# Kernel optimization log

Measured on AMD Instinct MI355X. Metric: run time of the kernel, lower is better.

The kernel has to match this reference:

```python
import jax, jax.numpy as jnp
import numpy as np

HIDDEN = 1024
N_HEADS = 16
HEAD_DIM = 64
LOCAL_WINDOW = 1024
GLOBAL_STRIDE = 512


def _sparse_mask(seq_len):
    # local sliding window (half-window each side), strided global columns, causal
    i = jnp.arange(seq_len)[:, None]
    j = jnp.arange(seq_len)[None, :]
    diff = i - j
    local = jnp.abs(diff) <= (LOCAL_WINDOW // 2)
    glob = (j % GLOBAL_STRIDE) == 0
    causal = diff >= 0
    return (local | glob) & causal  # [S, S] bool


def setup_inputs() -> dict:
    key = jax.random.key(0)
    k0, k1, k2, k3, k4 = jax.random.split(key, 5)
    B, S = 1, 2048
    scale = 1.0 / np.sqrt(HIDDEN)
    return {
        "hidden_states": jax.random.normal(k0, (B, S, HIDDEN), dtype=jnp.float32),
        "w_q": jax.random.normal(k1, (HIDDEN, N_HEADS * HEAD_DIM), dtype=jnp.float32) * scale,
        "w_k": jax.random.normal(k2, (HIDDEN, N_HEADS * HEAD_DIM), dtype=jnp.float32) * scale,
        "w_v": jax.random.normal(k3, (HIDDEN, N_HEADS * HEAD_DIM), dtype=jnp.float32) * scale,
        "w_o": jax.random.normal(k4, (N_HEADS * HEAD_DIM, HIDDEN), dtype=jnp.float32) * scale,
    }


def reference(hidden_states, w_q, w_k, w_v, w_o):
    B, S, _ = hidden_states.shape

    def shape(x):  # [B,S,H*D] -> [B,H,S,D]
        return x.reshape(B, S, N_HEADS, HEAD_DIM).transpose(0, 2, 1, 3)

    q = shape(hidden_states @ w_q)
    k = shape(hidden_states @ w_k)
    v = shape(hidden_states @ w_v)

    scores = jnp.einsum("bhqd,bhkd->bhqk", q, k) / np.sqrt(HEAD_DIM)
    mask = _sparse_mask(S)  # [S,S]
    scores = jnp.where(mask[None, None], scores, -jnp.inf)
    attn = jax.nn.softmax(scores, axis=-1)
    out = jnp.einsum("bhqk,bhkd->bhqd", attn, v)
    out = out.transpose(0, 2, 1, 3).reshape(B, S, N_HEADS * HEAD_DIM)
    return out @ w_o
```

## Files before the change

### kernel.cpp

```cpp
#include <hip/hip_runtime.h>

#define SEQ 2048
#define HID 1024
#define NH 16
#define HD 64
#define QKVLD 3072

typedef __attribute__((ext_vector_type(8))) short bf16x8;
typedef __attribute__((ext_vector_type(4))) float f32x4;

__device__ __forceinline__ unsigned short f2bf(float f) {
  unsigned int x = __float_as_uint(f);
  x += 0x7fffu + ((x >> 16) & 1u);
  return (unsigned short)(x >> 16);
}

__device__ __forceinline__ float bf2f(unsigned short u) {
  return __uint_as_float(((unsigned int)u) << 16);
}

__device__ __forceinline__ void gld_lds16(const void* g, void* l) {
  __builtin_amdgcn_global_load_lds((__attribute__((address_space(1))) void*)g,
                                   (__attribute__((address_space(3))) void*)l, 16, 0, 0);
}

__global__ void prep(const float* __restrict__ X, const float* __restrict__ Wq,
                     const float* __restrict__ Wk, const float* __restrict__ Wv,
                     const float* __restrict__ Wo, unsigned short* __restrict__ Xb,
                     unsigned short* __restrict__ WtQKV, unsigned short* __restrict__ WtO) {
  const int z = blockIdx.z;
  if (z == 4) {
    int bid = blockIdx.y * 32 + blockIdx.x;
    int t = threadIdx.y * 32 + threadIdx.x;
    size_t base = (size_t)bid * 2048 + t * 4;
#pragma unroll
    for (int half = 0; half < 2; half++) {
      float4 v = *(const float4*)(X + base + half * 1024);
      ushort4 o;
      o.x = f2bf(v.x); o.y = f2bf(v.y); o.z = f2bf(v.z); o.w = f2bf(v.w);
      *(ushort4*)(Xb + base + half * 1024) = o;
    }
    return;
  }
  __shared__ float tile[32][33];
  const float* S = (z == 0) ? Wq : (z == 1) ? Wk : (z == 2) ? Wv : Wo;
  unsigned short* D = (z < 3) ? (WtQKV + (size_t)z * HID * HID) : WtO;
  const float scale = (z == 0) ? 0.125f : 1.0f;
  int r0 = blockIdx.y * 32, c0 = blockIdx.x * 32;
  int tx = threadIdx.x, ty = threadIdx.y;
#pragma unroll
  for (int k = 0; k < 4; k++)
    tile[ty + k * 8][tx] = S[(size_t)(r0 + ty + k * 8) * HID + c0 + tx];
  __syncthreads();
#pragma unroll
  for (int k = 0; k < 4; k++)
    D[(size_t)(c0 + ty + k * 8) * HID + r0 + tx] = f2bf(scale * tile[tx][ty + k * 8]);
}

template <int MI, int BN, int GX, int RW, int OUT>
__global__ __launch_bounds__(256, 2) void gemm_bt(const unsigned short* __restrict__ A,
                                                  const unsigned short* __restrict__ Bt,
                                                  void* __restrict__ Cout,
                                                  unsigned short* __restrict__ Vout,
                                                  int M, int N, int K) {
  constexpr int NI = BN / 32;
  constexpr int TM = MI * 32;
  __shared__ unsigned short As[TM * 128];
  __shared__ unsigned short Bs[BN * 128];
  const int tid = threadIdx.x;
  const int lane = tid & 63;
  const int w = tid >> 6;
  const int wm = w >> 1, wn = w & 1;
  const int quad = lane >> 4, l16 = lane & 15;

  const int lin = blockIdx.x + GX * blockIdx.y;
  const int xcd = lin & 7, idx = lin >> 3;
  const int bx = (xcd & 3) * RW + (idx % RW);
  const int by = (xcd >> 2) * (64 / RW) + (idx / RW);
  const int bm = by * TM, bn = bx * BN;

  f32x4 acc[MI][NI] = {};

  for (int k0 = 0; k0 < K; k0 += 128) {
#pragma unroll
    for (int c = tid; c < TM * 16; c += 256) {
      int r = c >> 4, kc = c & 15;
      int g = (kc & 12) + ((kc & 3) ^ (r & 3));
      gld_lds16(A + (size_t)(bm + r) * K + k0 + g * 8, As + c * 8);
    }
#pragma unroll
    for (int c = tid; c < BN * 16; c += 256) {
      int r = c >> 4, kc = c & 15;
      int g = (kc & 12) + ((kc & 3) ^ (r & 3));
      gld_lds16(Bt + (size_t)(bn + r) * K + k0 + g * 8, Bs + c * 8);
    }
    __syncthreads();
#pragma unroll
    for (int ks = 0; ks < 4; ks++) {
      bf16x8 af[MI], bfr[NI];
#pragma unroll
      for (int mi = 0; mi < MI; mi++) {
        int m = wm * (MI * 16) + mi * 16 + l16;
        af[mi] = *(const bf16x8*)(As + (m * 16 + ks * 4 + (quad ^ (m & 3))) * 8);
      }
#pragma unroll
      for (int ni = 0; ni < NI; ni++) {
        int n = wn * (BN / 2) + ni * 16 + l16;
        bfr[ni] = *(const bf16x8*)(Bs + (n * 16 + ks * 4 + (quad ^ (n & 3))) * 8);
      }
#pragma unroll
      for (int mi = 0; mi < MI; mi++)
#pragma unroll
        for (int ni = 0; ni < NI; ni++)
          acc[mi][ni] = __builtin_amdgcn_mfma_f32_16x16x32_bf16(af[mi], bfr[ni], acc[mi][ni], 0, 0, 0);
    }
    __syncthreads();
  }

#pragma unroll
  for (int mi = 0; mi < MI; mi++) {
#pragma unroll
    for (int ni = 0; ni < NI; ni++) {
      int row = bm + wm * (MI * 16) + mi * 16 + quad * 4;
      int col = bn + wn * (BN / 2) + ni * 16 + l16;
      if (OUT == 0) {
#pragma unroll
        for (int r = 0; r < 4; r++)
          ((float*)Cout)[(size_t)(row + r) * N + col] = acc[mi][ni][r];
      } else {
        if (col < 2 * HID) {
#pragma unroll
          for (int r = 0; r < 4; r++)
            ((unsigned short*)Cout)[(size_t)(row + r) * N + col] = f2bf(acc[mi][ni][r]);
        } else {
          ushort4 o;
          o.x = f2bf(acc[mi][ni][0]); o.y = f2bf(acc[mi][ni][1]);
          o.z = f2bf(acc[mi][ni][2]); o.w = f2bf(acc[mi][ni][3]);
          *(ushort4*)(Vout + (size_t)(col - 2 * HID) * SEQ + row) = o;
        }
      }
    }
  }
}

__global__ __launch_bounds__(256, 4) void attn_sparse(const unsigned short* __restrict__ QKV,
                                                      const unsigned short* __restrict__ VtG,
                                                      unsigned short* __restrict__ AttO) {
  __shared__ unsigned short Ks[64 * 64];
  __shared__ unsigned short Vt[64 * 64];
  __shared__ unsigned short Pw[4][16 * 72];
  const int lin = blockIdx.x + 32 * blockIdx.y;
  const int xcd = lin & 7, slot = lin >> 3;
  const int h = slot >> 2;
  const int qbase = (xcd * 4 + (slot & 3)) * 64;
  const int tid = threadIdx.x;
  const int lane = tid & 63, w = tid >> 6;
  const int quad = lane >> 4, l16 = lane & 15;
  const int qrow0 = qbase + w * 16;
  unsigned short* pws = &Pw[w][0];

  bf16x8 aq[2];
  {
    const unsigned short* qp = QKV + (size_t)(qrow0 + l16) * QKVLD + h * HD + quad * 8;
    aq[0] = *(const bf16x8*)qp;
    aq[1] = *(const bf16x8*)(qp + 32);
  }

  f32x4 accO[4] = {};
  float lsum = 0.f;

  const int jlo = (qbase >= 512) ? (qbase - 512) : 0;
  const int ng = (jlo > 0) ? ((jlo + 511) >> 9) : 0;
  const int ntl = ((qbase - jlo) >> 6) + 1;

  for (int t = 0; t < ntl; t++) {
    const int j0 = jlo + t * 64;
    if (t > 0) __syncthreads();
#pragma unroll
    for (int c = tid; c < 512; c += 256) {
      int r = c >> 3, kc = c & 7;
      int g = (kc & 4) + ((kc & 3) ^ (r & 3));
      gld_lds16(QKV + (size_t)(j0 + r) * QKVLD + HID + h * HD + g * 8, Ks + c * 8);
      gld_lds16(VtG + (size_t)(h * HD + r) * SEQ + j0 + g * 8, Vt + c * 8);
    }
    __syncthreads();

    f32x4 s[4] = {};
#pragma unroll
    for (int nj = 0; nj < 4; nj++) {
      int row = nj * 16 + l16;
#pragma unroll
      for (int ks = 0; ks < 2; ks++) {
        bf16x8 ak = *(const bf16x8*)(Ks + (row * 8 + ks * 4 + (quad ^ (row & 3))) * 8);
        s[nj] = __builtin_amdgcn_mfma_f32_16x16x32_bf16(ak, aq[ks], s[nj], 0, 0, 0);
      }
    }

    const bool isdiag = (t == ntl - 1);
    const bool istrail = (t == 0) && (qbase >= 512);
    const int trailg = (istrail && ((j0 & 511) == 0)) ? 1 : 0;
    const int db = qrow0 + l16 - j0 - quad * 4;
#pragma unroll
    for (int nj = 0; nj < 4; nj++) {
      float p[4];
#pragma unroll
      for (int r = 0; r < 4; r++) {
        float x = fminf(s[nj][r], 60.0f);
        int d = db - nj * 16 - r;
        bool valid = true;
        if (isdiag) valid = (d >= 0);
        else if (istrail) valid = (d <= 512) || (trailg && (nj * 16 + quad * 4 + r) == 0);
        x = valid ? x : -1e30f;
        p[r] = __expf(x);
        lsum += p[r];
      }
      unsigned int u01 = (unsigned)f2bf(p[0]) | ((unsigned)f2bf(p[1]) << 16);
      unsigned int u23 = (unsigned)f2bf(p[2]) | ((unsigned)f2bf(p[3]) << 16);
      *(uint2*)(pws + l16 * 72 + nj * 16 + quad * 4) = make_uint2(u01, u23);
    }

#pragma unroll
    for (int kk = 0; kk < 2; kk++) {
      bf16x8 bp = *(const bf16x8*)(pws + l16 * 72 + kk * 32 + quad * 8);
#pragma unroll
      for (int nd = 0; nd < 4; nd++) {
        int row = nd * 16 + l16;
        bf16x8 av = *(const bf16x8*)(Vt + (row * 8 + kk * 4 + (quad ^ (row & 3))) * 8);
        accO[nd] = __builtin_amdgcn_mfma_f32_16x16x32_bf16(av, bp, accO[nd], 0, 0, 0);
      }
    }
  }

  if (ng > 0) {
    __syncthreads();
    if (tid < ng * 8) {
      int r = tid >> 3, kc = tid & 7;
      int g = (kc & 4) + ((kc & 3) ^ (r & 3));
      *(uint4*)(Ks + tid * 8) =
          *(const uint4*)(QKV + ((size_t)r << 9) * QKVLD + HID + h * HD + g * 8);
    }
    if (tid < ng * 64) {
      int d = tid & 63, c = tid >> 6;
      Vt[(d * 8 + (d & 3)) * 8 + c] = VtG[(size_t)(h * HD + d) * SEQ + ((size_t)c << 9)];
    }
    __syncthreads();
    f32x4 s0 = {};
#pragma unroll
    for (int ks = 0; ks < 2; ks++) {
      bf16x8 ak = *(const bf16x8*)(Ks + (l16 * 8 + ks * 4 + (quad ^ (l16 & 3))) * 8);
      s0 = __builtin_amdgcn_mfma_f32_16x16x32_bf16(ak, aq[ks], s0, 0, 0, 0);
    }
    float p[4];
#pragma unroll
    for (int r = 0; r < 4; r++) {
      p[r] = ((quad * 4 + r) < ng) ? __expf(fminf(s0[r], 60.0f)) : 0.f;
      lsum += p[r];
    }
    unsigned int u01 = (unsigned)f2bf(p[0]) | ((unsigned)f2bf(p[1]) << 16);
    unsigned int u23 = (unsigned)f2bf(p[2]) | ((unsigned)f2bf(p[3]) << 16);
    *(uint2*)(pws + l16 * 72 + quad * 4) = make_uint2(u01, u23);
    *(uint2*)(pws + l16 * 72 + 16 + quad * 4) = make_uint2(0, 0);
    bf16x8 bp = *(const bf16x8*)(pws + l16 * 72 + quad * 8);
#pragma unroll
    for (int nd = 0; nd < 4; nd++) {
      int row = nd * 16 + l16;
      bf16x8 av = *(const bf16x8*)(Vt + (row * 8 + (quad ^ (row & 3))) * 8);
      accO[nd] = __builtin_amdgcn_mfma_f32_16x16x32_bf16(av, bp, accO[nd], 0, 0, 0);
    }
  }

  lsum += __shfl_xor(lsum, 16);
  lsum += __shfl_xor(lsum, 32);
  const float rl = 1.0f / lsum;
  const int i = qrow0 + l16;
#pragma unroll
  for (int nd = 0; nd < 4; nd++) {
    ushort4 o;
    o.x = f2bf(accO[nd][0] * rl);
    o.y = f2bf(accO[nd][1] * rl);
    o.z = f2bf(accO[nd][2] * rl);
    o.w = f2bf(accO[nd][3] * rl);
    *(ushort4*)(AttO + (size_t)i * HID + h * HD + nd * 16 + quad * 4) = o;
  }
}

extern "C" void kernel_launch(void* const* d_in, const int* in_sizes, int n_in,
                              void* d_out, int out_size, void* d_ws, size_t ws_size,
                              hipStream_t stream) {
  const float* X  = (const float*)d_in[0];
  const float* Wq = (const float*)d_in[1];
  const float* Wk = (const float*)d_in[2];
  const float* Wv = (const float*)d_in[3];
  const float* Wo = (const float*)d_in[4];
  float* out = (float*)d_out;

  unsigned short* Xb    = (unsigned short*)d_ws;
  unsigned short* WtQKV = Xb + (size_t)SEQ * HID;
  unsigned short* WtO   = WtQKV + (size_t)QKVLD * HID;
  unsigned short* QKV   = WtO + (size_t)HID * HID;
  unsigned short* VtG   = QKV + (size_t)SEQ * QKVLD;
  unsigned short* AttO  = VtG + (size_t)HID * SEQ;

  prep<<<dim3(32, 32, 5), dim3(32, 8), 0, stream>>>(X, Wq, Wk, Wv, Wo, Xb, WtQKV, WtO);

  gemm_bt<4, 96, 32, 8, 2><<<dim3(32, 16), dim3(256), 0, stream>>>(
      Xb, WtQKV, QKV, VtG, SEQ, QKVLD, HID);

  attn_sparse<<<dim3(SEQ / 64, NH), dim3(256), 0, stream>>>(QKV, VtG, AttO);

  gemm_bt<2, 64, 16, 4, 0><<<dim3(16, 32), dim3(256), 0, stream>>>(
      AttO, WtO, out, nullptr, SEQ, HID, HID);
}
```

Before: 128.4 us.

## Double-buffer K/V tiles in sparse attention and use packed bf16 conversion

The sparse attention kernel now keeps two LDS buffers for K and V and issues the async global-to-LDS loads for the next tile before computing on the current one, so load latency can overlap with the MFMA work. That needs double the K/V shared memory, and launch bounds drop from 4 to 3 blocks per CU to match. Manual bf16 rounding is replaced with the packed __float22bfloat162_rn intrinsic in several places, and the fminf clamp before exp is removed. The loop-end sync has no matching wait on the async loads, so correctness depends on how the compiler orders that memory traffic, and a stray self-assignment to Ks[0][0] was added.

```diff
diff --git a/kernel.cpp b/kernel.cpp
--- a/kernel.cpp
+++ b/kernel.cpp
@@ -1,4 +1,5 @@
 #include <hip/hip_runtime.h>
+#include <hip/hip_bf16.h>
 
 #define SEQ 2048
 #define HID 1024
@@ -15,8 +16,10 @@
   return (unsigned short)(x >> 16);
 }
 
-__device__ __forceinline__ float bf2f(unsigned short u) {
-  return __uint_as_float(((unsigned int)u) << 16);
+__device__ __forceinline__ unsigned int pkbf(float a, float b) {
+  union { __hip_bfloat162 h2; unsigned int u; } cvt;
+  cvt.h2 = __float22bfloat162_rn(make_float2(a, b));
+  return cvt.u;
 }
 
 __device__ __forceinline__ void gld_lds16(const void* g, void* l) {
@@ -36,9 +39,7 @@
 #pragma unroll
     for (int half = 0; half < 2; half++) {
       float4 v = *(const float4*)(X + base + half * 1024);
-      ushort4 o;
-      o.x = f2bf(v.x); o.y = f2bf(v.y); o.z = f2bf(v.z); o.w = f2bf(v.w);
-      *(ushort4*)(Xb + base + half * 1024) = o;
+      *(uint2*)(Xb + base + half * 1024) = make_uint2(pkbf(v.x, v.y), pkbf(v.z, v.w));
     }
     return;
   }
@@ -133,21 +134,20 @@
           for (int r = 0; r < 4; r++)
             ((unsigned short*)Cout)[(size_t)(row + r) * N + col] = f2bf(acc[mi][ni][r]);
         } else {
-          ushort4 o;
-          o.x = f2bf(acc[mi][ni][0]); o.y = f2bf(acc[mi][ni][1]);
-          o.z = f2bf(acc[mi][ni][2]); o.w = f2bf(acc[mi][ni][3]);
-          *(ushort4*)(Vout + (size_t)(col - 2 * HID) * SEQ + row) = o;
+          *(uint2*)(Vout + (size_t)(col - 2 * HID) * SEQ + row) =
+              make_uint2(pkbf(acc[mi][ni][0], acc[mi][ni][1]),
+                         pkbf(acc[mi][ni][2], acc[mi][ni][3]));
         }
       }
     }
   }
 }
 
-__global__ __launch_bounds__(256, 4) void attn_sparse(const unsigned short* __restrict__ QKV,
+__global__ __launch_bounds__(256, 3) void attn_sparse(const unsigned short* __restrict__ QKV,
                                                       const unsigned short* __restrict__ VtG,
                                                       unsigned short* __restrict__ AttO) {
-  __shared__ unsigned short Ks[64 * 64];
-  __shared__ unsigned short Vt[64 * 64];
+  __shared__ unsigned short Ks[2][64 * 64];
+  __shared__ unsigned short Vt[2][64 * 64];
   __shared__ unsigned short Pw[4][16 * 72];
   const int lin = blockIdx.x + 32 * blockIdx.y;
   const int xcd = lin & 7, slot = lin >> 3;
@@ -173,17 +173,24 @@
   const int ng = (jlo > 0) ? ((jlo + 511) >> 9) : 0;
   const int ntl = ((qbase - jlo) >> 6) + 1;
 
-  for (int t = 0; t < ntl; t++) {
-    const int j0 = jlo + t * 64;
-    if (t > 0) __syncthreads();
+  auto stage = [&](int j0, int b) {
 #pragma unroll
     for (int c = tid; c < 512; c += 256) {
       int r = c >> 3, kc = c & 7;
       int g = (kc & 4) + ((kc & 3) ^ (r & 3));
-      gld_lds16(QKV + (size_t)(j0 + r) * QKVLD + HID + h * HD + g * 8, Ks + c * 8);
-      gld_lds16(VtG + (size_t)(h * HD + r) * SEQ + j0 + g * 8, Vt + c * 8);
-    }
-    __syncthreads();
+      gld_lds16(QKV + (size_t)(j0 + r) * QKVLD + HID + h * HD + g * 8, &Ks[b][c * 8]);
+      gld_lds16(VtG + (size_t)(h * HD + r) * SEQ + j0 + g * 8, &Vt[b][c * 8]);
+    }
+  };
+
+  stage(jlo, 0);
+  __syncthreads();
+
+  for (int t = 0; t < ntl; t++) {
+    if (t + 1 < ntl) stage(jlo + (t + 1) * 64, (t + 1) & 1);
+    const unsigned short* KsB = Ks[t & 1];
+    const unsigned short* VtB = Vt[t & 1];
+    const int j0 = jlo + t * 64;
 
     f32x4 s[4] = {};
 #pragma unroll
@@ -191,7 +198,7 @@
       int row = nj * 16 + l16;
 #pragma unroll
       for (int ks = 0; ks < 2; ks++) {
-        bf16x8 ak = *(const bf16x8*)(Ks + (row * 8 + ks * 4 + (quad ^ (row & 3))) * 8);
+        bf16x8 ak = *(const bf16x8*)(KsB + (row * 8 + ks * 4 + (quad ^ (row & 3))) * 8);
         s[nj] = __builtin_amdgcn_mfma_f32_16x16x32_bf16(ak, aq[ks], s[nj], 0, 0, 0);
       }
     }
@@ -205,7 +212,7 @@
       float p[4];
 #pragma unroll
       for (int r = 0; r < 4; r++) {
-        float x = fminf(s[nj][r], 60.0f);
+        float x = s[nj][r];
         int d = db - nj * 16 - r;
         bool valid = true;
         if (isdiag) valid = (d >= 0);
@@ -214,9 +221,8 @@
         p[r] = __expf(x);
         lsum += p[r];
       }
-      unsigned int u01 = (unsigned)f2bf(p[0]) | ((unsigned)f2bf(p[1]) << 16);
-      unsigned int u23 = (unsigned)f2bf(p[2]) | ((unsigned)f2bf(p[3]) << 16);
-      *(uint2*)(pws + l16 * 72 + nj * 16 + quad * 4) = make_uint2(u01, u23);
+      *(uint2*)(pws + l16 * 72 + nj * 16 + quad * 4) =
+          make_uint2(pkbf(p[0], p[1]), pkbf(p[2], p[3]));
     }
 
 #pragma unroll
@@ -225,46 +231,45 @@
 #pragma unroll
       for (int nd = 0; nd < 4; nd++) {
         int row = nd * 16 + l16;
-        bf16x8 av = *(const bf16x8*)(Vt + (row * 8 + kk * 4 + (quad ^ (row & 3))) * 8);
+        bf16x8 av = *(const bf16x8*)(VtB + (row * 8 + kk * 4 + (quad ^ (row & 3))) * 8);
         accO[nd] = __builtin_amdgcn_mfma_f32_16x16x32_bf16(av, bp, accO[nd], 0, 0, 0);
       }
     }
+    __syncthreads();
   }
 
   if (ng > 0) {
-    __syncthreads();
     if (tid < ng * 8) {
       int r = tid >> 3, kc = tid & 7;
       int g = (kc & 4) + ((kc & 3) ^ (r & 3));
-      *(uint4*)(Ks + tid * 8) =
+      *(uint4*)(&Ks[0][tid * 8]) =
           *(const uint4*)(QKV + ((size_t)r << 9) * QKVLD + HID + h * HD + g * 8);
     }
     if (tid < ng * 64) {
       int d = tid & 63, c = tid >> 6;
-      Vt[(d * 8 + (d & 3)) * 8 + c] = VtG[(size_t)(h * HD + d) * SEQ + ((size_t)c << 9)];
+      Ks[0][0] = Ks[0][0];
+      Vt[0][(d * 8 + (d & 3)) * 8 + c] = VtG[(size_t)(h * HD + d) * SEQ + ((size_t)c << 9)];
     }
     __syncthreads();
     f32x4 s0 = {};
 #pragma unroll
     for (int ks = 0; ks < 2; ks++) {
-      bf16x8 ak = *(const bf16x8*)(Ks + (l16 * 8 + ks * 4 + (quad ^ (l16 & 3))) * 8);
+      bf16x8 ak = *(const bf16x8*)(&Ks[0][(l16 * 8 + ks * 4 + (quad ^ (l16 & 3))) * 8]);
       s0 = __builtin_amdgcn_mfma_f32_16x16x32_bf16(ak, aq[ks], s0, 0, 0, 0);
     }
     float p[4];
 #pragma unroll
     for (int r = 0; r < 4; r++) {
-      p[r] = ((quad * 4 + r) < ng) ? __expf(fminf(s0[r], 60.0f)) : 0.f;
+      p[r] = ((quad * 4 + r) < ng) ? __expf(s0[r]) : 0.f;
       lsum += p[r];
     }
-    unsigned int u01 = (unsigned)f2bf(p[0]) | ((unsigned)f2bf(p[1]) << 16);
-    unsigned int u23 = (unsigned)f2bf(p[2]) | ((unsigned)f2bf(p[3]) << 16);
-    *(uint2*)(pws + l16 * 72 + quad * 4) = make_uint2(u01, u23);
+    *(uint2*)(pws + l16 * 72 + quad * 4) = make_uint2(pkbf(p[0], p[1]), pkbf(p[2], p[3]));
     *(uint2*)(pws + l16 * 72 + 16 + quad * 4) = make_uint2(0, 0);
     bf16x8 bp = *(const bf16x8*)(pws + l16 * 72 + quad * 8);
 #pragma unroll
     for (int nd = 0; nd < 4; nd++) {
       int row = nd * 16 + l16;
-      bf16x8 av = *(const bf16x8*)(Vt + (row * 8 + (quad ^ (row & 3))) * 8);
+      bf16x8 av = *(const bf16x8*)(&Vt[0][(row * 8 + (quad ^ (row & 3))) * 8]);
       accO[nd] = __builtin_amdgcn_mfma_f32_16x16x32_bf16(av, bp, accO[nd], 0, 0, 0);
     }
   }
@@ -275,12 +280,9 @@
   const int i = qrow0 + l16;
 #pragma unroll
   for (int nd = 0; nd < 4; nd++) {
-    ushort4 o;
-    o.x = f2bf(accO[nd][0] * rl);
-    o.y = f2bf(accO[nd][1] * rl);
-    o.z = f2bf(accO[nd][2] * rl);
-    o.w = f2bf(accO[nd][3] * rl);
-    *(ushort4*)(AttO + (size_t)i * HID + h * HD + nd * 16 + quad * 4) = o;
+    *(uint2*)(AttO + (size_t)i * HID + h * HD + nd * 16 + quad * 4) =
+        make_uint2(pkbf(accO[nd][0] * rl, accO[nd][1] * rl),
+                   pkbf(accO[nd][2] * rl, accO[nd][3] * rl));
   }
 }
 
```

Measured after the change: 127.8 us. No clear change (-0.5%).
